# Performance work log

Hardware: AMD Instinct MI355X
Metric: run time of the kernel (lower is better)

## Reference

```python
import jax, jax.numpy as jnp
import numpy as np
from math import comb

H, W = 256, 256          # canvas_shape
S = 15                   # num_samples along each bezier curve
EPS = 1e-6


def _bezier_samples(key_points):
    # key_points: [B, K, 2] in pixel coords. Uniform-t Bernstein evaluation.
    K = key_points.shape[1]
    ts = jnp.linspace(0.0, 1.0, S)                              # [S]
    k = jnp.arange(K)
    binom = jnp.asarray([comb(K - 1, i) for i in range(K)], dtype=key_points.dtype)
    basis = binom * ts[:, None] ** k * (1.0 - ts[:, None]) ** (K - 1 - k)  # [S, K]
    return jnp.einsum('sk,bkd->bsd', basis, key_points)         # [B, S, 2]


def setup_inputs() -> dict:
    key = jax.random.key(0)
    k1, k2, k3 = jax.random.split(key, 3)
    inputs = jax.random.uniform(k1, (64, 4, 2), dtype=jnp.float32)          # normalized (y, x)
    widths = jax.random.uniform(k2, (64,), dtype=jnp.float32) * 19.0 + 1.0  # 1..20 px
    aa_factors = jax.random.uniform(k3, (64,), dtype=jnp.float32) * 2.0 + 0.5
    return {"inputs": inputs, "widths": widths, "aa_factors": aa_factors}


def reference(inputs, widths, aa_factors):
    B = inputs.shape[0]
    canvas_shape = jnp.asarray([H, W], dtype=inputs.dtype)
    key_points = inputs * canvas_shape                 # [B, K, 2]
    sample_points = _bezier_samples(key_points)        # [B, S, 2]

    # positions built as [[y, x] for x in range(W) for y in range(H)] -> x-major flatten
    ys = jnp.tile(jnp.arange(H), W)
    xs = jnp.repeat(jnp.arange(W), H)
    positions = jnp.stack([ys, xs], axis=1).astype(inputs.dtype)   # [P, 2], P = H*W

    diff = positions[None, None, :, :] - sample_points[:, :, None, :]  # [B, S, P, 2]
    distances = jnp.sqrt(jnp.sum(diff * diff, axis=-1))                # [B, S, P]
    min_dist = jnp.min(distances, axis=1)                              # [B, P]

    canvas = (min_dist / widths[:, None] + EPS) ** aa_factors[:, None]
    canvas = jnp.clip(1.0 - canvas, 0.0, 1.0)
    return canvas.reshape(B, H, W)
```

## Files before the change

### kernel.cpp

```cpp
#include <hip/hip_runtime.h>

#define HH 256
#define WW 256
#define SS 15
#define NB 64

__device__ __forceinline__ float alog2(float x) {
    float r; asm("v_log_f32 %0, %1" : "=v"(r) : "v"(x)); return r;
}
__device__ __forceinline__ float aexp2(float x) {
    float r; asm("v_exp_f32 %0, %1" : "=v"(r) : "v"(x)); return r;
}

__global__ __launch_bounds__(256) void CurveGraphic2d_kernel(
    const float* __restrict__ inputs,
    const float* __restrict__ widths,
    const float* __restrict__ aaf,
    float* __restrict__ out)
{
    const int blocksPerBatch = (HH * WW) / 1024;
    const int b     = blockIdx.x / blocksPerBatch;
    const int chunk = blockIdx.x % blocksPerBatch;
    const int tid   = threadIdx.x;

    __shared__ float spy[SS];
    __shared__ float spx[SS];

    if (tid < SS) {
        float t = (float)tid * (1.0f / (float)(SS - 1));
        float u = 1.0f - t;
        float b0 = u * u * u;
        float b1 = 3.0f * t * u * u;
        float b2 = 3.0f * t * t * u;
        float b3 = t * t * t;
        const float* kp = inputs + b * 8;
        spy[tid] = 256.0f * (b0 * kp[0] + b1 * kp[2] + b2 * kp[4] + b3 * kp[6]);
        spx[tid] = 256.0f * (b0 * kp[1] + b1 * kp[3] + b2 * kp[5] + b3 * kp[7]);
    }
    __syncthreads();

    const float w  = widths[b];
    const float af = aaf[b];
    const float haf   = 0.5f * af;
    const float cbias = -af * log2f(w);

    const int base = chunk * 1024 + tid * 4;
    const int i = base >> 8;
    const int j = base & 255;
    const float x  = (float)i;
    const float y0 = (float)j;

    float m0 = 1e30f, m1 = 1e30f, m2 = 1e30f, m3 = 1e30f;
    #pragma unroll
    for (int s = 0; s < SS; ++s) {
        float dx  = x - spx[s];
        float dxx = dx * dx;
        float sy  = spy[s];
        float dy0 = y0          - sy;
        float dy1 = (y0 + 1.0f) - sy;
        float dy2 = (y0 + 2.0f) - sy;
        float dy3 = (y0 + 3.0f) - sy;
        m0 = fminf(m0, fmaf(dy0, dy0, dxx));
        m1 = fminf(m1, fmaf(dy1, dy1, dxx));
        m2 = fminf(m2, fmaf(dy2, dy2, dxx));
        m3 = fminf(m3, fmaf(dy3, dy3, dxx));
    }

    float4 o;
    {
        float p;
        p   = aexp2(fmaf(haf, alog2(m0), cbias));
        o.x = fminf(fmaxf(1.0f - p, 0.0f), 1.0f);
        p   = aexp2(fmaf(haf, alog2(m1), cbias));
        o.y = fminf(fmaxf(1.0f - p, 0.0f), 1.0f);
        p   = aexp2(fmaf(haf, alog2(m2), cbias));
        o.z = fminf(fmaxf(1.0f - p, 0.0f), 1.0f);
        p   = aexp2(fmaf(haf, alog2(m3), cbias));
        o.w = fminf(fmaxf(1.0f - p, 0.0f), 1.0f);
    }

    *reinterpret_cast<float4*>(out + (size_t)b * (HH * WW) + base) = o;
}

extern "C" void kernel_launch(void* const* d_in, const int* in_sizes, int n_in,
                              void* d_out, int out_size, void* d_ws, size_t ws_size,
                              hipStream_t stream) {
    const float* inputs = (const float*)d_in[0];
    const float* widths = (const float*)d_in[1];
    const float* aaf    = (const float*)d_in[2];
    float* out = (float*)d_out;

    const int blocks = NB * ((HH * WW) / 1024);
    CurveGraphic2d_kernel<<<blocks, 256, 0, stream>>>(inputs, widths, aaf, out);
}
```

Baseline: 12.64 us.

## Compute 4x4 pixel tiles per thread and skip samples beyond stroke width

Each thread now computes a 4x4 block of pixels instead of 4 pixels in a row, reusing per-sample x distances across columns and cutting the grid to a quarter of the blocks. Samples whose squared x-distance exceeds the squared width are skipped, because such pixels would clamp to zero anyway. Sample points are packed into a float2 shared array. This adds branches and more registers per thread and reduces the number of waves available for latency hiding.

```diff
diff --git a/kernel.cpp b/kernel.cpp
--- a/kernel.cpp
+++ b/kernel.cpp
@@ -18,13 +18,13 @@
     const float* __restrict__ aaf,
     float* __restrict__ out)
 {
-    const int blocksPerBatch = (HH * WW) / 1024;
-    const int b     = blockIdx.x / blocksPerBatch;
-    const int chunk = blockIdx.x % blocksPerBatch;
-    const int tid   = threadIdx.x;
+    const int b      = blockIdx.x >> 4;
+    const int blk    = blockIdx.x & 15;
+    const int tid    = threadIdx.x;
+    const int lane   = tid & 63;
+    const int region = blk * 4 + (tid >> 6);
 
-    __shared__ float spy[SS];
-    __shared__ float spx[SS];
+    __shared__ float2 sp[SS];
 
     if (tid < SS) {
         float t = (float)tid * (1.0f / (float)(SS - 1));
@@ -34,52 +34,78 @@
         float b2 = 3.0f * t * t * u;
         float b3 = t * t * t;
         const float* kp = inputs + b * 8;
-        spy[tid] = 256.0f * (b0 * kp[0] + b1 * kp[2] + b2 * kp[4] + b3 * kp[6]);
-        spx[tid] = 256.0f * (b0 * kp[1] + b1 * kp[3] + b2 * kp[5] + b3 * kp[7]);
+        float syv = 256.0f * (b0 * kp[0] + b1 * kp[2] + b2 * kp[4] + b3 * kp[6]);
+        float sxv = 256.0f * (b0 * kp[1] + b1 * kp[3] + b2 * kp[5] + b3 * kp[7]);
+        sp[tid] = make_float2(syv, sxv);
     }
     __syncthreads();
 
     const float w  = widths[b];
-    const float af = aaf[b];
+    const float w2 = w * w;
+
+    const float x0 = (float)(region * 4);
+    const float y0 = (float)(lane * 4);
+
+    float m[4][4];
+    #pragma unroll
+    for (int c = 0; c < 4; ++c)
+        #pragma unroll
+        for (int k = 0; k < 4; ++k) m[c][k] = 1e30f;
+
+    #pragma unroll
+    for (int s = 0; s < SS; ++s) {
+        float2 pp  = sp[s];
+        float sys  = pp.x, sxs = pp.y;
+        float d0   = x0 - sxs;
+        float d1   = d0 + 1.0f, d2 = d0 + 2.0f, d3 = d0 + 3.0f;
+        float dxx0 = d0 * d0, dxx1 = d1 * d1, dxx2 = d2 * d2, dxx3 = d3 * d3;
+        float mn   = fminf(fminf(dxx0, dxx1), fminf(dxx2, dxx3));
+        if (mn < w2) {
+            float dy0 = y0 - sys;
+            float dy1 = dy0 + 1.0f, dy2 = dy0 + 2.0f, dy3 = dy0 + 3.0f;
+            float q0 = dy0 * dy0, q1 = dy1 * dy1, q2 = dy2 * dy2, q3 = dy3 * dy3;
+            if (dxx0 < w2) {
+                m[0][0] = fminf(m[0][0], q0 + dxx0);
+                m[0][1] = fminf(m[0][1], q1 + dxx0);
+                m[0][2] = fminf(m[0][2], q2 + dxx0);
+                m[0][3] = fminf(m[0][3], q3 + dxx0);
+            }
+            if (dxx1 < w2) {
+                m[1][0] = fminf(m[1][0], q0 + dxx1);
+                m[1][1] = fminf(m[1][1], q1 + dxx1);
+                m[1][2] = fminf(m[1][2], q2 + dxx1);
+                m[1][3] = fminf(m[1][3], q3 + dxx1);
+            }
+            if (dxx2 < w2) {
+                m[2][0] = fminf(m[2][0], q0 + dxx2);
+                m[2][1] = fminf(m[2][1], q1 + dxx2);
+                m[2][2] = fminf(m[2][2], q2 + dxx2);
+                m[2][3] = fminf(m[2][3], q3 + dxx2);
+            }
+            if (dxx3 < w2) {
+                m[3][0] = fminf(m[3][0], q0 + dxx3);
+                m[3][1] = fminf(m[3][1], q1 + dxx3);
+                m[3][2] = fminf(m[3][2], q2 + dxx3);
+                m[3][3] = fminf(m[3][3], q3 + dxx3);
+            }
+        }
+    }
+
+    const float af    = aaf[b];
     const float haf   = 0.5f * af;
     const float cbias = -af * log2f(w);
 
-    const int base = chunk * 1024 + tid * 4;
-    const int i = base >> 8;
-    const int j = base & 255;
-    const float x  = (float)i;
-    const float y0 = (float)j;
+    float* dst = out + (size_t)b * (HH * WW) + region * 1024 + lane * 4;
 
-    float m0 = 1e30f, m1 = 1e30f, m2 = 1e30f, m3 = 1e30f;
     #pragma unroll
-    for (int s = 0; s < SS; ++s) {
-        float dx  = x - spx[s];
-        float dxx = dx * dx;
-        float sy  = spy[s];
-        float dy0 = y0          - sy;
-        float dy1 = (y0 + 1.0f) - sy;
-        float dy2 = (y0 + 2.0f) - sy;
-        float dy3 = (y0 + 3.0f) - sy;
-        m0 = fminf(m0, fmaf(dy0, dy0, dxx));
-        m1 = fminf(m1, fmaf(dy1, dy1, dxx));
-        m2 = fminf(m2, fmaf(dy2, dy2, dxx));
-        m3 = fminf(m3, fmaf(dy3, dy3, dxx));
+    for (int c = 0; c < 4; ++c) {
+        float4 o;
+        o.x = fmaxf(1.0f - aexp2(fmaf(haf, alog2(m[c][0]), cbias)), 0.0f);
+        o.y = fmaxf(1.0f - aexp2(fmaf(haf, alog2(m[c][1]), cbias)), 0.0f);
+        o.z = fmaxf(1.0f - aexp2(fmaf(haf, alog2(m[c][2]), cbias)), 0.0f);
+        o.w = fmaxf(1.0f - aexp2(fmaf(haf, alog2(m[c][3]), cbias)), 0.0f);
+        *reinterpret_cast<float4*>(dst + c * 256) = o;
     }
-
-    float4 o;
-    {
-        float p;
-        p   = aexp2(fmaf(haf, alog2(m0), cbias));
-        o.x = fminf(fmaxf(1.0f - p, 0.0f), 1.0f);
-        p   = aexp2(fmaf(haf, alog2(m1), cbias));
-        o.y = fminf(fmaxf(1.0f - p, 0.0f), 1.0f);
-        p   = aexp2(fmaf(haf, alog2(m2), cbias));
-        o.z = fminf(fmaxf(1.0f - p, 0.0f), 1.0f);
-        p   = aexp2(fmaf(haf, alog2(m3), cbias));
-        o.w = fminf(fmaxf(1.0f - p, 0.0f), 1.0f);
-    }
-
-    *reinterpret_cast<float4*>(out + (size_t)b * (HH * WW) + base) = o;
 }
 
 extern "C" void kernel_launch(void* const* d_in, const int* in_sizes, int n_in,
@@ -90,6 +116,6 @@
     const float* aaf    = (const float*)d_in[2];
     float* out = (float*)d_out;
 
-    const int blocks = NB * ((HH * WW) / 1024);
+    const int blocks = NB * 16;
     CurveGraphic2d_kernel<<<blocks, 256, 0, stream>>>(inputs, widths, aaf, out);
 }
```

Result: slower. 14.01 us (+10.8%).
